# Kernel tuning notes

Measured on AMD Instinct MI355X. Metric: run time of the kernel, lower is better.

The kernel has to match this reference:

```python
import jax, jax.numpy as jnp
import numpy as np

# pywt db4 decomposition filters (dec_lo, dec_hi), 8 taps
DEC_LO = np.array([-0.010597401784997278, 0.032883011666982945, 0.030841381835986965,
                   -0.18703481171888114, -0.02798376941698385, 0.6308807679295904,
                   0.7148465705525415, 0.23037781330885523], dtype=np.float32)
DEC_HI = np.array([-0.23037781330885523, 0.7148465705525415, -0.6308807679295904,
                   -0.02798376941698385, 0.18703481171888114, 0.030841381835986965,
                   -0.032883011666982945, -0.010597401784997278], dtype=np.float32)
FLEN = 8
LEVELS = 5


def _dwt_level(x):
    """Single-level DWT matching pywt.dwt(x, 'db4', mode='symmetric').

    x: [N, L] -> (cA, cD) each [N, (L + FLEN - 1) // 2]
    Equivalent to: ext = symmetric pad by FLEN-1 each side;
    np.convolve(ext, filt, 'valid')[1::2].
    """
    ext = jnp.pad(x, ((0, 0), (FLEN - 1, FLEN - 1)), mode='symmetric')
    ext = ext[:, 1:]  # offset so stride-2 hits full-conv positions 1,3,5,...
    # true convolution == lax cross-correlation with reversed filter
    k = jnp.stack([jnp.asarray(DEC_LO, x.dtype)[::-1],
                   jnp.asarray(DEC_HI, x.dtype)[::-1]])[:, None, :]  # [2,1,F]
    y = jax.lax.conv_general_dilated(ext[:, None, :], k,
                                     window_strides=(2,), padding='VALID')
    return y[:, 0, :], y[:, 1, :]


def setup_inputs() -> dict:
    key = jax.random.key(0)
    x = jax.random.normal(key, (64, 64, 4096), dtype=jnp.float32)
    return {"x": x}


def reference(x):
    B, C, T = x.shape
    a = x.reshape(B * C, T)
    details = []  # cD1, cD2, ..., cD5 (finest first)
    for _ in range(LEVELS):
        a, d = _dwt_level(a)
        details.append(d)
    approx = a.reshape(B, C, -1)
    # module returns details ordered coarsest-first: [cD5, cD4, ..., cD1]
    detail_coeffs = [d.reshape(B, C, -1) for d in details[::-1]]
    return (approx, *detail_coeffs)
```

## Files before the change

kernel.cpp:

```cpp
#include <hip/hip_runtime.h>

#define T0 4096
#define N1 2051
#define BLOCK 256
#define PAD 6

#define RLO0  0.23037781330885523f
#define RLO1  0.7148465705525415f
#define RLO2  0.6308807679295904f
#define RLO3 -0.02798376941698385f
#define RLO4 -0.18703481171888114f
#define RLO5  0.030841381835986965f
#define RLO6  0.032883011666982945f
#define RLO7 -0.010597401784997278f

#define RHI0 -0.010597401784997278f
#define RHI1 -0.032883011666982945f
#define RHI2  0.030841381835986965f
#define RHI3  0.18703481171888114f
#define RHI4 -0.02798376941698385f
#define RHI5 -0.6308807679295904f
#define RHI6  0.7148465705525415f
#define RHI7 -0.23037781330885523f

__device__ __forceinline__ int symidx(int t, int L) {
    t = (t < 0) ? (-1 - t) : t;
    t = (t >= L) ? (2 * L - 1 - t) : t;
    return t;
}

__device__ __forceinline__ void filt8(const float* __restrict__ t,
                                      float& lo, float& hi) {
    lo = RLO0 * t[0];            hi = RHI0 * t[0];
    lo = fmaf(RLO1, t[1], lo);   hi = fmaf(RHI1, t[1], hi);
    lo = fmaf(RLO2, t[2], lo);   hi = fmaf(RHI2, t[2], hi);
    lo = fmaf(RLO3, t[3], lo);   hi = fmaf(RHI3, t[3], hi);
    lo = fmaf(RLO4, t[4], lo);   hi = fmaf(RHI4, t[4], hi);
    lo = fmaf(RLO5, t[5], lo);   hi = fmaf(RHI5, t[5], hi);
    lo = fmaf(RLO6, t[6], lo);   hi = fmaf(RHI6, t[6], hi);
    lo = fmaf(RLO7, t[7], lo);   hi = fmaf(RHI7, t[7], hi);
}

__global__ __launch_bounds__(BLOCK) void dwt5_kernel(
    const float* __restrict__ x, float* __restrict__ out,
    long long offA, long long offD1, long long offD2, long long offD3,
    long long offD4, long long offD5)
{
    __shared__ float extB[N1 + 16];
    __shared__ float extC[1029 + 16];

    const int row = blockIdx.x;
    const int tid = threadIdx.x;
    const float* __restrict__ xrow = x + (size_t)row * T0;
    float* __restrict__ d1 = out + offD1 + (long long)row * N1;

    float2 t[8][4];
    {
        const int b0 = (tid >= 3) ? (2 * tid - 6) : 0;
        const float2* __restrict__ p = reinterpret_cast<const float2*>(xrow + b0);
#pragma unroll
        for (int q = 0; q < 4; ++q) t[0][q] = p[q];
    }
#pragma unroll
    for (int k = 1; k < 8; ++k) {
        const float2* __restrict__ p =
            reinterpret_cast<const float2*>(xrow + 2 * (tid + 256 * k) - 6);
#pragma unroll
        for (int q = 0; q < 4; ++q) t[k][q] = p[q];
    }

#pragma unroll
    for (int k = 0; k < 8; ++k) {
        const int i = tid + 256 * k;
        const float tt[8] = {t[k][0].x, t[k][0].y, t[k][1].x, t[k][1].y,
                             t[k][2].x, t[k][2].y, t[k][3].x, t[k][3].y};
        float lo, hi;
        filt8(tt, lo, hi);
        __builtin_nontemporal_store(hi, &d1[i]);
        extB[PAD + i] = lo;
        if (i < 6)       extB[5 - i] = lo;
        if (i >= N1 - 7) extB[PAD + N1 + (N1 - 1 - i)] = lo;
    }

    if (tid < 3) {
        {
            const int i = tid;
            float tt[8];
#pragma unroll
            for (int k = 0; k < 8; ++k) tt[k] = xrow[symidx(2 * i - 6 + k, T0)];
            float lo, hi;
            filt8(tt, lo, hi);
            __builtin_nontemporal_store(hi, &d1[i]);
            extB[PAD + i] = lo;
            extB[5 - i] = lo;
        }
        {
            const int i = 2048 + tid;
            float tt[8];
#pragma unroll
            for (int k = 0; k < 8; ++k) tt[k] = xrow[symidx(2 * i - 6 + k, T0)];
            float lo, hi;
            filt8(tt, lo, hi);
            __builtin_nontemporal_store(hi, &d1[i]);
            extB[PAD + i] = lo;
            extB[PAD + N1 + (N1 - 1 - i)] = lo;
        }
    }
    __syncthreads();

    const long long dOff[4] = {offD2, offD3, offD4, offD5};
    float* src = extB;
    float* dst = extC;
    int L = N1;
#pragma unroll
    for (int lev = 0; lev < 4; ++lev) {
        const int nOut = (L + 7) >> 1;
        float* __restrict__ dSeg = out + dOff[lev] + (long long)row * nOut;
        float* __restrict__ aSeg = out + offA + (long long)row * nOut;
        const float2* __restrict__ e2 = reinterpret_cast<const float2*>(src);
        for (int i = tid; i < nOut; i += BLOCK) {
            const float2 w0 = e2[i + 0];
            const float2 w1 = e2[i + 1];
            const float2 w2 = e2[i + 2];
            const float2 w3 = e2[i + 3];
            const float tt[8] = {w0.x, w0.y, w1.x, w1.y, w2.x, w2.y, w3.x, w3.y};
            float lo, hi;
            filt8(tt, lo, hi);
            __builtin_nontemporal_store(hi, &dSeg[i]);
            if (lev == 3) {
                __builtin_nontemporal_store(lo, &aSeg[i]);
            } else {
                dst[PAD + i] = lo;
                if (i < 6)         dst[5 - i] = lo;
                if (i >= nOut - 7) dst[PAD + nOut + (nOut - 1 - i)] = lo;
            }
        }
        __syncthreads();
        float* tmp = src; src = dst; dst = tmp;
        L = nOut;
    }
}

extern "C" void kernel_launch(void* const* d_in, const int* in_sizes, int n_in,
                              void* d_out, int out_size, void* d_ws, size_t ws_size,
                              hipStream_t stream) {
    const float* x = (const float*)d_in[0];
    float* out = (float*)d_out;

    const int rows = in_sizes[0] / T0;
    const int n1 = (T0 + 7) / 2;
    const int n2 = (n1 + 7) / 2;
    const int n3 = (n2 + 7) / 2;
    const int n4 = (n3 + 7) / 2;
    const int n5 = (n4 + 7) / 2;

    const long long offA  = 0;
    const long long offD5 = offA  + (long long)rows * n5;
    const long long offD4 = offD5 + (long long)rows * n5;
    const long long offD3 = offD4 + (long long)rows * n4;
    const long long offD2 = offD3 + (long long)rows * n3;
    const long long offD1 = offD2 + (long long)rows * n2;

    dwt5_kernel<<<rows, BLOCK, 0, stream>>>(x, out, offA, offD1, offD2, offD3,
                                            offD4, offD5);
}
```

Measured before the change: 111.5 us.

## Buffer all detail outputs in registers and store them after the final level

Detail coefficients from every level are kept in registers and written to global memory together at the end of the kernel, instead of being stored as each level is computed. The level loop is fully unrolled with compile-time sizes, which removes the dynamic strided loops. The aim is to keep stores off the critical path between the LDS stages and to group them into one burst. The cost is higher register pressure, which may lower occupancy, and stores can no longer overlap with the later levels' compute.

```diff
diff --git a/kernel.cpp b/kernel.cpp
--- a/kernel.cpp
+++ b/kernel.cpp
@@ -2,6 +2,10 @@
 
 #define T0 4096
 #define N1 2051
+#define N2 1029
+#define N3 518
+#define N4 262
+#define N5 134
 #define BLOCK 256
 #define PAD 6
 
@@ -47,12 +51,11 @@
     long long offD4, long long offD5)
 {
     __shared__ float extB[N1 + 16];
-    __shared__ float extC[1029 + 16];
+    __shared__ float extC[N2 + 16];
 
     const int row = blockIdx.x;
     const int tid = threadIdx.x;
     const float* __restrict__ xrow = x + (size_t)row * T0;
-    float* __restrict__ d1 = out + offD1 + (long long)row * N1;
 
     float2 t[8][4];
     {
@@ -69,6 +72,7 @@
         for (int q = 0; q < 4; ++q) t[k][q] = p[q];
     }
 
+    float d1r[8];
 #pragma unroll
     for (int k = 0; k < 8; ++k) {
         const int i = tid + 256 * k;
@@ -76,21 +80,21 @@
                              t[k][2].x, t[k][2].y, t[k][3].x, t[k][3].y};
         float lo, hi;
         filt8(tt, lo, hi);
-        __builtin_nontemporal_store(hi, &d1[i]);
+        d1r[k] = hi;
         extB[PAD + i] = lo;
         if (i < 6)       extB[5 - i] = lo;
         if (i >= N1 - 7) extB[PAD + N1 + (N1 - 1 - i)] = lo;
     }
 
+    float fixL = 0.f, fixR = 0.f;
     if (tid < 3) {
         {
             const int i = tid;
             float tt[8];
 #pragma unroll
             for (int k = 0; k < 8; ++k) tt[k] = xrow[symidx(2 * i - 6 + k, T0)];
-            float lo, hi;
-            filt8(tt, lo, hi);
-            __builtin_nontemporal_store(hi, &d1[i]);
+            float lo;
+            filt8(tt, lo, fixL);
             extB[PAD + i] = lo;
             extB[5 - i] = lo;
         }
@@ -99,45 +103,118 @@
             float tt[8];
 #pragma unroll
             for (int k = 0; k < 8; ++k) tt[k] = xrow[symidx(2 * i - 6 + k, T0)];
-            float lo, hi;
-            filt8(tt, lo, hi);
-            __builtin_nontemporal_store(hi, &d1[i]);
+            float lo;
+            filt8(tt, lo, fixR);
             extB[PAD + i] = lo;
             extB[PAD + N1 + (N1 - 1 - i)] = lo;
         }
     }
     __syncthreads();
 
-    const long long dOff[4] = {offD2, offD3, offD4, offD5};
-    float* src = extB;
-    float* dst = extC;
-    int L = N1;
-#pragma unroll
-    for (int lev = 0; lev < 4; ++lev) {
-        const int nOut = (L + 7) >> 1;
-        float* __restrict__ dSeg = out + dOff[lev] + (long long)row * nOut;
-        float* __restrict__ aSeg = out + offA + (long long)row * nOut;
-        const float2* __restrict__ e2 = reinterpret_cast<const float2*>(src);
-        for (int i = tid; i < nOut; i += BLOCK) {
-            const float2 w0 = e2[i + 0];
-            const float2 w1 = e2[i + 1];
-            const float2 w2 = e2[i + 2];
-            const float2 w3 = e2[i + 3];
-            const float tt[8] = {w0.x, w0.y, w1.x, w1.y, w2.x, w2.y, w3.x, w3.y};
-            float lo, hi;
-            filt8(tt, lo, hi);
-            __builtin_nontemporal_store(hi, &dSeg[i]);
-            if (lev == 3) {
-                __builtin_nontemporal_store(lo, &aSeg[i]);
-            } else {
-                dst[PAD + i] = lo;
-                if (i < 6)         dst[5 - i] = lo;
-                if (i >= nOut - 7) dst[PAD + nOut + (nOut - 1 - i)] = lo;
+    float r2[5];
+    {
+        const float2* __restrict__ e2 = reinterpret_cast<const float2*>(extB);
+#pragma unroll
+        for (int s = 0; s < 5; ++s) {
+            const int i = tid + 256 * s;
+            if (s < 4 || tid < 5) {
+                const float2 w0 = e2[i], w1 = e2[i + 1], w2 = e2[i + 2], w3 = e2[i + 3];
+                const float tt[8] = {w0.x, w0.y, w1.x, w1.y, w2.x, w2.y, w3.x, w3.y};
+                float lo, hi;
+                filt8(tt, lo, hi);
+                r2[s] = hi;
+                extC[PAD + i] = lo;
+                if (i < 6)       extC[5 - i] = lo;
+                if (i >= N2 - 7) extC[PAD + N2 + (N2 - 1 - i)] = lo;
             }
         }
-        __syncthreads();
-        float* tmp = src; src = dst; dst = tmp;
-        L = nOut;
+    }
+    __syncthreads();
+
+    float r3[3];
+    {
+        const float2* __restrict__ e2 = reinterpret_cast<const float2*>(extC);
+#pragma unroll
+        for (int s = 0; s < 3; ++s) {
+            const int i = tid + 256 * s;
+            if (s < 2 || tid < 6) {
+                const float2 w0 = e2[i], w1 = e2[i + 1], w2 = e2[i + 2], w3 = e2[i + 3];
+                const float tt[8] = {w0.x, w0.y, w1.x, w1.y, w2.x, w2.y, w3.x, w3.y};
+                float lo, hi;
+                filt8(tt, lo, hi);
+                r3[s] = hi;
+                extB[PAD + i] = lo;
+                if (i < 6)       extB[5 - i] = lo;
+                if (i >= N3 - 7) extB[PAD + N3 + (N3 - 1 - i)] = lo;
+            }
+        }
+    }
+    __syncthreads();
+
+    float r4[2];
+    {
+        const float2* __restrict__ e2 = reinterpret_cast<const float2*>(extB);
+#pragma unroll
+        for (int s = 0; s < 2; ++s) {
+            const int i = tid + 256 * s;
+            if (s < 1 || tid < 6) {
+                const float2 w0 = e2[i], w1 = e2[i + 1], w2 = e2[i + 2], w3 = e2[i + 3];
+                const float tt[8] = {w0.x, w0.y, w1.x, w1.y, w2.x, w2.y, w3.x, w3.y};
+                float lo, hi;
+                filt8(tt, lo, hi);
+                r4[s] = hi;
+                extC[PAD + i] = lo;
+                if (i < 6)       extC[5 - i] = lo;
+                if (i >= N4 - 7) extC[PAD + N4 + (N4 - 1 - i)] = lo;
+            }
+        }
+    }
+    __syncthreads();
+
+    float r5 = 0.f, rA = 0.f;
+    if (tid < N5) {
+        const float2* __restrict__ e2 = reinterpret_cast<const float2*>(extC);
+        const int i = tid;
+        const float2 w0 = e2[i], w1 = e2[i + 1], w2 = e2[i + 2], w3 = e2[i + 3];
+        const float tt[8] = {w0.x, w0.y, w1.x, w1.y, w2.x, w2.y, w3.x, w3.y};
+        filt8(tt, rA, r5);
+    }
+
+    float* __restrict__ d1 = out + offD1 + (long long)row * N1;
+    float* __restrict__ d2 = out + offD2 + (long long)row * N2;
+    float* __restrict__ d3 = out + offD3 + (long long)row * N3;
+    float* __restrict__ d4 = out + offD4 + (long long)row * N4;
+    float* __restrict__ d5 = out + offD5 + (long long)row * N5;
+    float* __restrict__ aO = out + offA  + (long long)row * N5;
+
+#pragma unroll
+    for (int k = 0; k < 8; ++k) {
+        const int i = tid + 256 * k;
+        if (k > 0 || tid >= 3)
+            __builtin_nontemporal_store(d1r[k], &d1[i]);
+    }
+    if (tid < 3) {
+        __builtin_nontemporal_store(fixL, &d1[tid]);
+        __builtin_nontemporal_store(fixR, &d1[2048 + tid]);
+    }
+#pragma unroll
+    for (int s = 0; s < 5; ++s) {
+        const int i = tid + 256 * s;
+        if (s < 4 || tid < 5) __builtin_nontemporal_store(r2[s], &d2[i]);
+    }
+#pragma unroll
+    for (int s = 0; s < 3; ++s) {
+        const int i = tid + 256 * s;
+        if (s < 2 || tid < 6) __builtin_nontemporal_store(r3[s], &d3[i]);
+    }
+#pragma unroll
+    for (int s = 0; s < 2; ++s) {
+        const int i = tid + 256 * s;
+        if (s < 1 || tid < 6) __builtin_nontemporal_store(r4[s], &d4[i]);
+    }
+    if (tid < N5) {
+        __builtin_nontemporal_store(r5, &d5[tid]);
+        __builtin_nontemporal_store(rA, &aO[tid]);
     }
 }
 
@@ -148,18 +225,13 @@
     float* out = (float*)d_out;
 
     const int rows = in_sizes[0] / T0;
-    const int n1 = (T0 + 7) / 2;
-    const int n2 = (n1 + 7) / 2;
-    const int n3 = (n2 + 7) / 2;
-    const int n4 = (n3 + 7) / 2;
-    const int n5 = (n4 + 7) / 2;
 
     const long long offA  = 0;
-    const long long offD5 = offA  + (long long)rows * n5;
-    const long long offD4 = offD5 + (long long)rows * n5;
-    const long long offD3 = offD4 + (long long)rows * n4;
-    const long long offD2 = offD3 + (long long)rows * n3;
-    const long long offD1 = offD2 + (long long)rows * n2;
+    const long long offD5 = offA  + (long long)rows * N5;
+    const long long offD4 = offD5 + (long long)rows * N5;
+    const long long offD3 = offD4 + (long long)rows * N4;
+    const long long offD2 = offD3 + (long long)rows * N3;
+    const long long offD1 = offD2 + (long long)rows * N2;
 
     dwt5_kernel<<<rows, BLOCK, 0, stream>>>(x, out, offA, offD1, offD2, offD3,
                                             offD4, offD5);
```

Result: no change. 112.3 us (+0.8%).
